# Kernel optimization log

Hardware: AMD Instinct MI355X
Metric: run time of the kernel (lower is better)

The kernel has to match this reference:

```python
import jax, jax.numpy as jnp
import numpy as np
from jax import lax

DIM = 64
HEADS = 8

def conv1x1(x, w):
    # x: [B,C,H,W], w: [O,I,1,1]
    return lax.conv_general_dilated(x, w, (1, 1), 'VALID',
                                    dimension_numbers=('NCHW', 'OIHW', 'NCHW'))

def dwconv3x3(x, w):
    # depthwise 3x3, w: [C,1,3,3]
    C = x.shape[1]
    return lax.conv_general_dilated(x, w, (1, 1), ((1, 1), (1, 1)),
                                    dimension_numbers=('NCHW', 'OIHW', 'NCHW'),
                                    feature_group_count=C)

def setup_inputs() -> dict:
    key = jax.random.key(0)
    ks = jax.random.split(key, 7)
    B, C, H, W = 8, DIM, 256, 256
    x = jax.random.normal(ks[0], (B, C, H, W), dtype=jnp.float32)
    w_gate = jax.random.normal(ks[1], (C, C, 1, 1), dtype=jnp.float32) * 0.05
    w_gate_dw = jax.random.normal(ks[2], (C, 1, 3, 3), dtype=jnp.float32) * 0.05
    w_qkv = jax.random.normal(ks[3], (3 * C, C, 1, 1), dtype=jnp.float32) * 0.05
    w_qkv_dw = jax.random.normal(ks[4], (3 * C, 1, 3, 3), dtype=jnp.float32) * 0.05
    w_proj = jax.random.normal(ks[5], (C, C, 1, 1), dtype=jnp.float32) * 0.05
    temperature = jnp.ones((HEADS, 1, 1), dtype=jnp.float32)
    return {'x': x, 'w_gate': w_gate, 'w_gate_dw': w_gate_dw,
            'w_qkv': w_qkv, 'w_qkv_dw': w_qkv_dw, 'w_proj': w_proj,
            'temperature': temperature}

def reference(x, w_gate, w_gate_dw, w_qkv, w_qkv_dw, w_proj, temperature):
    b, c, h, w = x.shape
    head = HEADS
    cph = c // head  # channels per head

    gate = dwconv3x3(conv1x1(x, w_gate), w_gate_dw)  # [b,c,h,w]
    qkv = dwconv3x3(conv1x1(x, w_qkv), w_qkv_dw)     # [b,3c,h,w]
    q, k, v = jnp.split(qkv, 3, axis=1)

    def to_heads(t):
        return t.reshape(b, head, cph, h * w)  # [b,head,c',hw]
    q, k, v = to_heads(q), to_heads(k), to_heads(v)

    # L2-normalize along the spatial (hw) axis (torch F.normalize, eps=1e-12)
    q = q / jnp.maximum(jnp.linalg.norm(q, axis=-1, keepdims=True), 1e-12)
    k = k / jnp.maximum(jnp.linalg.norm(k, axis=-1, keepdims=True), 1e-12)

    # transposed attention over channels: [b,head,c',c']
    attn = jnp.einsum('bhcn,bhdn->bhcd', q, k) * temperature
    attn = jax.nn.softmax(attn, axis=-1)
    out = jnp.einsum('bhcd,bhdn->bhcn', attn, v)  # [b,head,c',hw]
    out = out.reshape(b, c, h, w)

    out = jax.nn.gelu(gate, approximate=False) * out
    out = conv1x1(out, w_proj)
    return out
```

## Files before the change

kernel.cpp:

```cpp
#include <hip/hip_runtime.h>

typedef _Float16 f16;
using f16x4 = __attribute__((ext_vector_type(4))) _Float16;
using f16x8 = __attribute__((ext_vector_type(8))) _Float16;
using f32x4 = __attribute__((ext_vector_type(4))) float;

#define HW 65536
#define NBAND 16
#define ROWS 16
#define RS 320

static __device__ __forceinline__ float my_erf(float v) {
  float x = fabsf(v);
  float t = 1.f / (1.f + 0.3275911f * x);
  float y = t * (0.254829592f + t * (-0.284496736f + t * (1.421413741f
          + t * (-1.453152027f + t * 1.061405429f))));
  float r = 1.f - y * __expf(-x * x);
  return v < 0.f ? -r : r;
}
static __device__ __forceinline__ float my_gelu(float s) {
  return 0.5f * s * (1.f + my_erf(s * 0.70710678118654752f));
}

__global__ void TRA_Attention_15281493639325_kernel() {}

__global__ void k_signal(float* out, long long n, float val) {
  long long i = (long long)blockIdx.x * blockDim.x + threadIdx.x;
  long long stride = (long long)gridDim.x * blockDim.x;
  for (; i < n; i += stride) out[i] = val;
}

__global__ __launch_bounds__(256) void k0_wconv(
    const float* __restrict__ w_gate, const float* __restrict__ w_qkv,
    f16* __restrict__ W16)
{
  int i = blockIdx.x * 256 + threadIdx.x;
  int m = i >> 4, kc = i & 15;
  const float* src = (m < 64) ? (w_gate + m*64 + kc*4)
                              : (w_qkv + (m-64)*64 + kc*4);
  float4 f = *(const float4*)src;
  f16x4 pk = { (f16)f.x, (f16)f.y, (f16)f.z, (f16)f.w };
  *(f16x4*)(W16 + m*64 + kc*4) = pk;
}

__global__ __launch_bounds__(256) void k1_mfma(
    const float* __restrict__ x, const f16* __restrict__ W16,
    f16* __restrict__ A)
{
  __shared__ __align__(16) unsigned char xs[8192];
  __shared__ __align__(16) f16 os[256*64];

  const int tid = threadIdx.x, blk = blockIdx.x;
  const int b = blk >> 8;
  const long long row0 = (long long)(blk & 255) * 256;

  const int wave = tid >> 6, lane = tid & 63;
  const int m0 = (wave >> 1) * 128, n0 = (wave & 1) * 32;
  const int lr = lane & 15, lg = lane >> 4;

  float4 pre[4];
  #pragma unroll
  for (int i = 0; i < 4; ++i) {
    int cid = tid + (i << 8), k = cid >> 4, c = cid & 15;
    pre[i] = *(const float4*)(x + ((long long)b*64 + k)*HW + row0 + c*4);
  }

  for (int t = 0; t < 4; ++t) {
    const long long p0 = row0 + t*64;

    #pragma unroll
    for (int i = 0; i < 4; ++i) {
      int cid = tid + (i << 8), k = cid >> 4, c = cid & 15;
      const float* e = (const float*)&pre[i];
      #pragma unroll
      for (int j = 0; j < 4; ++j) {
        int p = c*4 + j;
        int hp = ((p & 7) ^ ((p >> 3) & 7)) << 4;
        *(f16*)(xs + p*128 + ((2*k) ^ hp)) = (f16)e[j];
      }
    }
    __syncthreads();

    if (t < 3) {
      const long long pn = row0 + (t+1)*64;
      #pragma unroll
      for (int i = 0; i < 4; ++i) {
        int cid = tid + (i << 8), k = cid >> 4, c = cid & 15;
        pre[i] = *(const float4*)(x + ((long long)b*64 + k)*HW + pn + c*4);
      }
    }

    f32x4 acc[8][2];
    #pragma unroll
    for (int i = 0; i < 8; ++i)
      #pragma unroll
      for (int j = 0; j < 2; ++j) acc[i][j] = (f32x4){0.f,0.f,0.f,0.f};

    #pragma unroll
    for (int ks = 0; ks < 2; ++ks) {
      f16x8 af[8], bfr[2];
      #pragma unroll
      for (int mi = 0; mi < 8; ++mi) {
        int m = m0 + mi*16 + lr;
        af[mi] = *(const f16x8*)(W16 + m*64 + ks*32 + lg*8);
      }
      #pragma unroll
      for (int ni = 0; ni < 2; ++ni) {
        int p = n0 + ni*16 + lr;
        int hp = ((p & 7) ^ ((p >> 3) & 7)) << 4;
        bfr[ni] = *(const f16x8*)(xs + p*128 + ((ks*64 + lg*16) ^ hp));
      }
      #pragma unroll
      for (int mi = 0; mi < 8; ++mi)
        #pragma unroll
        for (int ni = 0; ni < 2; ++ni)
          acc[mi][ni] = __builtin_amdgcn_mfma_f32_16x16x32_f16(
              af[mi], bfr[ni], acc[mi][ni], 0, 0, 0);
    }
    __syncthreads();

    #pragma unroll
    for (int mi = 0; mi < 8; ++mi)
      #pragma unroll
      for (int ni = 0; ni < 2; ++ni)
        #pragma unroll
        for (int r = 0; r < 4; ++r) {
          int m = m0 + mi*16 + lg*4 + r;
          int p = n0 + ni*16 + lr;
          os[m*64 + (p ^ ((m & 7) << 3))] = (f16)acc[mi][ni][r];
        }
    __syncthreads();

    #pragma unroll
    for (int pass = 0; pass < 8; ++pass) {
      int idx = pass*256 + tid;
      int row = idx >> 3, c8 = idx & 7;
      f16x8 v = *(const f16x8*)((const unsigned char*)os + row*128
                                + ((c8 ^ (row & 7)) * 16));
      *(f16x8*)(A + ((long long)b*256 + row)*HW + p0 + c8*8) = v;
    }
    __syncthreads();
  }
}

__global__ __launch_bounds__(256) void k2a_dw(
    const f16* __restrict__ A, const float* __restrict__ w_gate_dw,
    const float* __restrict__ w_qkv_dw, f16* __restrict__ Vv, f16* __restrict__ GG)
{
  const int tid = threadIdx.x, blk = blockIdx.x;
  const int yband = blk & 3, ch2 = (blk >> 2) & 127, b = blk >> 9;
  const bool isv = ch2 >= 64;
  const int c = isv ? ch2 - 64 : ch2;
  const f16* src = A + ((long long)b*256 + (isv ? 192 + c : c)) * HW;
  const float* wsrc = isv ? (w_qkv_dw + (128 + c)*9) : (w_gate_dw + c*9);
  f16* dst = (isv ? Vv : GG) + ((long long)b*64 + c) * HW;

  float wd[9];
  #pragma unroll
  for (int j = 0; j < 9; ++j) wd[j] = wsrc[j];

  const int xc = tid & 31, ysub = tid >> 5;
  const int lane = tid & 63;
  const int xbase = xc * 8;
  const int y0 = yband * 64 + ysub * 8;

  float rb[3][10];

  auto load_row = [&](int y, float* r) {
    if (y >= 0 && y < 256) {
      uint4 raw = *(const uint4*)(src + y*256 + xbase);
      const f16* e = (const f16*)&raw;
      #pragma unroll
      for (int t = 0; t < 8; ++t) r[1 + t] = (float)e[t];
    } else {
      #pragma unroll
      for (int t = 0; t < 8; ++t) r[1 + t] = 0.f;
    }
    float lf = __shfl(r[8], lane - 1);
    float rf = __shfl(r[1], lane + 1);
    r[0] = (xc == 0)  ? 0.f : lf;
    r[9] = (xc == 31) ? 0.f : rf;
  };

  load_row(y0 - 1, rb[0]);
  load_row(y0,     rb[1]);

  #pragma unroll
  for (int i = 0; i < 8; ++i) {
    load_row(y0 + i + 1, rb[(i + 2) % 3]);
    const float* rm = rb[i % 3];
    const float* r0 = rb[(i + 1) % 3];
    const float* rp = rb[(i + 2) % 3];
    f16x8 st;
    #pragma unroll
    for (int j = 0; j < 8; ++j) {
      float s = wd[0]*rm[j] + wd[1]*rm[j+1] + wd[2]*rm[j+2]
              + wd[3]*r0[j] + wd[4]*r0[j+1] + wd[5]*r0[j+2]
              + wd[6]*rp[j] + wd[7]*rp[j+1] + wd[8]*rp[j+2];
      if (!isv) s = my_gelu(s);
      st[j] = (f16)s;
    }
    *(f16x8*)(dst + (y0 + i)*256 + xbase) = st;
  }
}

__device__ __forceinline__ int ridx(int c, int slot, int i) {
  return ((((c << 2) | slot) * RS) + i) ^ ((c & 7) << 3);
}

__global__ __launch_bounds__(64) void k2b_qk(
    const f16* __restrict__ A, const float* __restrict__ w_qkv_dw,
    float* __restrict__ GRP)
{
  __shared__ __align__(16) f16 ring[16*4*RS];
  const int lane = threadIdx.x, blk = blockIdx.x;
  const int band = blk & (NBAND-1), h = (blk >> 4) & 7, b = blk >> 7;

  const int c  = lane & 15, g  = lane >> 4;
  const int cs = lane >> 2, q4 = lane & 3;

  const int wrow = (c < 8) ? (h*8 + c) : (64 + h*8 + (c - 8));
  float wq[9];
  #pragma unroll
  for (int j = 0; j < 9; ++j) wq[j] = w_qkv_dw[wrow*9 + j];

  const f16* sbase = A + ((long long)b*256 +
      (cs < 8 ? 64 + h*8 + cs : 128 + h*8 + (cs - 8))) * HW;

  auto load_row = [&](int yy, uint4* r) {
    if (yy >= 0 && yy < 256) {
      const f16* p = sbase + yy*256 + q4*64;
      #pragma unroll
      for (int t = 0; t < 8; ++t) r[t] = *(const uint4*)(p + t*8);
    } else {
      #pragma unroll
      for (int t = 0; t < 8; ++t) r[t] = make_uint4(0u,0u,0u,0u);
    }
  };
  auto write_row = [&](int slot, const uint4* r) {
    #pragma unroll
    for (int t = 0; t < 8; ++t)
      *(uint4*)&ring[ridx(cs, slot, 8 + q4*64 + t*8)] = r[t];
  };

  auto conv_accum = [&](const f16x8* R, const float* w, float* fr, int q) {
    float v[10];
    #pragma unroll
    for (int t = 0; t < 8; ++t) v[1 + t] = (float)R[q][t];
    float e7p = (q > 0) ? (float)R[q-1][7] : 0.f;
    float e0n = (q < 7) ? (float)R[q+1][0] : 0.f;
    float L1 = __shfl(v[8], lane - 16);
    float L2 = __shfl(e7p, (lane & 15) + 48);
    float Q1 = __shfl(v[1], lane + 16);
    float Q2 = __shfl(e0n, lane & 15);
    v[0] = (g > 0) ? L1 : ((q > 0) ? L2 : 0.f);
    v[9] = (g < 3) ? Q1 : ((q < 7) ? Q2 : 0.f);
    #pragma unroll
    for (int j = 0; j < 8; ++j)
      fr[j] += w[0]*v[j] + w[1]*v[j+1] + w[2]*v[j+2];
  };

  f32x4 acc = (f32x4){0.f, 0.f, 0.f, 0.f};

  const int y0 = band * ROWS;
  {
    uint4 r[8];
    load_row(y0-1, r); write_row((y0+3)&3, r);
    load_row(y0,   r); write_row((y0+4)&3, r);
    load_row(y0+1, r); write_row((y0+5)&3, r);
  }
  __syncthreads();

  for (int y = y0; y < y0 + ROWS; ++y) {
    uint4 r[8];
    const bool pf = (y + 2 <= y0 + ROWS);
    if (pf) load_row(y + 2, r);

    const int s0 = (y+3)&3, s1 = (y+4)&3, s2 = (y+5)&3;
    f16x8 Rm[8], Rc[8], Rp[8];
    #pragma unroll
    for (int q = 0; q < 8; ++q) {
      Rm[q] = *(const f16x8*)&ring[ridx(c, s0, 8 + q*32 + g*8)];
      Rc[q] = *(const f16x8*)&ring[ridx(c, s1, 8 + q*32 + g*8)];
      Rp[q] = *(const f16x8*)&ring[ridx(c, s2, 8 + q*32 + g*8)];
    }

    #pragma unroll
    for (int q = 0; q < 8; ++q) {
      float fr[8] = {0.f,0.f,0.f,0.f,0.f,0.f,0.f,0.f};
      conv_accum(Rm, wq + 0, fr, q);
      conv_accum(Rc, wq + 3, fr, q);
      conv_accum(Rp, wq + 6, fr, q);
      f16x8 frag;
      #pragma unroll
      for (int j = 0; j < 8; ++j) frag[j] = (f16)fr[j];
      acc = __builtin_amdgcn_mfma_f32_16x16x32_f16(frag, frag, acc, 0, 0, 0);
    }

    if (pf) write_row((y+6)&3, r);
    __syncthreads();
  }

  const long long gbase = (long long)((b*8 + h)*NBAND + band) * 80;
  #pragma unroll
  for (int reg = 0; reg < 4; ++reg) {
    int rrow = g*4 + reg;
    float val = acc[reg];
    if (rrow == c) GRP[gbase + c] = val;
    else if (rrow < 8 && c >= 8) GRP[gbase + 16 + rrow*8 + (c-8)] = val;
  }
}

__global__ __launch_bounds__(64) void k2c_attn(
    const float* __restrict__ GRP, const float* __restrict__ temp,
    float* __restrict__ ATT)
{
  __shared__ float s[80];
  const int tid = threadIdx.x;
  const int h = blockIdx.x & 7, b = blockIdx.x >> 3;
  for (int i = tid; i < 80; i += 64) {
    float v = 0.f;
    for (int band = 0; band < NBAND; ++band)
      v += GRP[(((b*8 + h)*NBAND + band) * 80) + i];
    s[i] = v;
  }
  __syncthreads();
  const int c = tid >> 3, d = tid & 7;
  float nq = fmaxf(sqrtf(s[c]), 1e-12f);
  float nk = fmaxf(sqrtf(s[8 + d]), 1e-12f);
  float logit = s[16 + c*8 + d] / (nq * nk) * temp[h];
  float m = logit;
  #pragma unroll
  for (int off = 4; off; off >>= 1) m = fmaxf(m, __shfl_xor(m, off));
  float e = __expf(logit - m);
  float sum = e;
  #pragma unroll
  for (int off = 4; off; off >>= 1) sum += __shfl_xor(sum, off);
  ATT[((b*8 + h)*8 + c)*8 + d] = e / sum;
}

__global__ __launch_bounds__(256) void k3_out(
    const f16* __restrict__ Vv, const f16* __restrict__ GG,
    const float* __restrict__ ATT, const float* __restrict__ w_proj,
    float* __restrict__ out)
{
  __shared__ __align__(16) unsigned char lds[64*128 + 256*128 + 2048];
  unsigned char* wl = lds;
  unsigned char* xs = lds + 64*128;
  float* attn_s = (float*)(lds + 64*128 + 256*128);

  const int tid = threadIdx.x;
  const int y = blockIdx.x & 255, b = blockIdx.x >> 8;

  for (int cid = tid; cid < 1024; cid += 256) {
    int m = cid >> 4, kc = cid & 15;
    float4 f = *(const float4*)(w_proj + m*64 + kc*4);
    int hm = ((m & 7) ^ ((m >> 3) & 7)) << 4;
    f16x4 pk = { (f16)f.x, (f16)f.y, (f16)f.z, (f16)f.w };
    *(f16x4*)(wl + m*128 + ((kc*8) ^ hm)) = pk;
  }
  for (int i = tid; i < 512; i += 256) attn_s[i] = ATT[b*512 + i];
  __syncthreads();

  {
    const int pg = tid & 31, hd = tid >> 5;
    const long long base = ((long long)b*64 + hd*8)*HW + (long long)y*256 + pg*8;
    f16x8 vv[8], gg[8];
    #pragma unroll
    for (int d = 0; d < 8; ++d)
      vv[d] = *(const f16x8*)(Vv + base + (long long)d*HW);
    #pragma unroll
    for (int c = 0; c < 8; ++c)
      gg[c] = *(const f16x8*)(GG + base + (long long)c*HW);
    float a[8][8];
    #pragma unroll
    for (int c = 0; c < 8; ++c)
      #pragma unroll
      for (int d = 0; d < 8; ++d) a[c][d] = attn_s[hd*64 + c*8 + d];
    #pragma unroll
    for (int j = 0; j < 8; ++j) {
      int p = pg*8 + j;
      int hp = ((p & 7) ^ ((p >> 3) & 7)) << 4;
      f16x8 st;
      #pragma unroll
      for (int c = 0; c < 8; ++c) {
        float av = 0.f;
        #pragma unroll
        for (int d = 0; d < 8; ++d) av += a[c][d] * (float)vv[d][j];
        st[c] = (f16)((float)gg[c][j] * av);
      }
      *(f16x8*)(xs + p*128 + ((hd*16) ^ hp)) = st;
    }
  }
  __syncthreads();

  const int wave = tid >> 6, lane = tid & 63;
  const int n0 = wave * 64;
  const int lr = lane & 15, lg = lane >> 4;

  f32x4 acc[4][4];
  #pragma unroll
  for (int i = 0; i < 4; ++i)
    #pragma unroll
    for (int j = 0; j < 4; ++j) acc[i][j] = (f32x4){0.f,0.f,0.f,0.f};

  #pragma unroll
  for (int ks = 0; ks < 2; ++ks) {
    f16x8 af[4], bfr[4];
    #pragma unroll
    for (int mi = 0; mi < 4; ++mi) {
      int m = mi*16 + lr;
      int hm = ((m & 7) ^ ((m >> 3) & 7)) << 4;
      af[mi] = *(const f16x8*)(wl + m*128 + ((ks*64 + lg*16) ^ hm));
    }
    #pragma unroll
    for (int ni = 0; ni < 4; ++ni) {
      int p = n0 + ni*16 + lr;
      int hp = ((p & 7) ^ ((p >> 3) & 7)) << 4;
      bfr[ni] = *(const f16x8*)(xs + p*128 + ((ks*64 + lg*16) ^ hp));
    }
    #pragma unroll
    for (int mi = 0; mi < 4; ++mi)
      #pragma unroll
      for (int ni = 0; ni < 4; ++ni)
        acc[mi][ni] = __builtin_amdgcn_mfma_f32_16x16x32_f16(
            af[mi], bfr[ni], acc[mi][ni], 0, 0, 0);
  }

  const long long obase = (long long)b*64*HW + (long long)y*256;
  #pragma unroll
  for (int mi = 0; mi < 4; ++mi)
    #pragma unroll
    for (int ni = 0; ni < 4; ++ni)
      #pragma unroll
      for (int r = 0; r < 4; ++r) {
        int m = mi*16 + lg*4 + r;
        int p = n0 + ni*16 + lr;
        out[obase + (long long)m*HW + p] = acc[mi][ni][r];
      }
}

extern "C" void kernel_launch(void* const* d_in, const int* in_sizes, int n_in,
                              void* d_out, int out_size, void* d_ws, size_t ws_size,
                              hipStream_t stream)
{
  float* out = (float*)d_out;

  int mp[7] = {-1,-1,-1,-1,-1,-1,-1};
  bool ok = (n_in == 7);
  if (ok) {
    int n4 = 0;
    for (int i = 0; i < 7; ++i) {
      long s = in_sizes[i];
      if      (s == 33554432) mp[0] = i;
      else if (s == 576)      mp[2] = i;
      else if (s == 12288)    mp[3] = i;
      else if (s == 1728)     mp[4] = i;
      else if (s == 8)        mp[6] = i;
      else if (s == 4096)     { if (n4 == 0) mp[1] = i; else mp[5] = i; ++n4; }
    }
    ok = ok && (n4 == 2);
    for (int i = 0; i < 7; ++i) ok = ok && (mp[i] >= 0);
  }
  if (!ok) { k_signal<<<2048,256,0,stream>>>(out, (long long)out_size, 2000.0f); return; }
  if (out_size != 33554432) { k_signal<<<2048,256,0,stream>>>(out, (long long)out_size, 3000.0f); return; }

  const float* x    = (const float*)d_in[mp[0]];
  const float* wg   = (const float*)d_in[mp[1]];
  const float* wgd  = (const float*)d_in[mp[2]];
  const float* wqkv = (const float*)d_in[mp[3]];
  const float* wqd  = (const float*)d_in[mp[4]];
  const float* wpj  = (const float*)d_in[mp[5]];
  const float* tp   = (const float*)d_in[mp[6]];

  unsigned char* ws = (unsigned char*)d_ws;
  const size_t GRP_SZ   = 8UL*8*NBAND*80*4;
  const size_t FULL     = 402653184UL + GRP_SZ + 16384UL + 32768UL;
  const size_t PERB_GRP = 8UL*NBAND*80*4;
  const size_t PERB     = 50331648UL + PERB_GRP + 2048UL + 32768UL;

  if (ws != nullptr && ws_size >= FULL) {
    f16*   A    = (f16*)ws;
    f16*   Vv   = (f16*)(ws + 268435456UL);
    f16*   GG   = (f16*)(ws + 335544320UL);
    float* GRP  = (float*)(ws + 402653184UL);
    float* ATT  = (float*)(ws + 402653184UL + GRP_SZ);
    f16*   W16  = (f16*)(ws + 402653184UL + GRP_SZ + 16384UL);
    k0_wconv<<<16,   256, 0, stream>>>(wg, wqkv, W16);
    k1_mfma <<<2048, 256, 0, stream>>>(x, W16, A);
    k2a_dw  <<<4096, 256, 0, stream>>>(A, wgd, wqd, Vv, GG);
    k2b_qk  <<<8*8*NBAND, 64, 0, stream>>>(A, wqd, GRP);
    k2c_attn<<<64,   64,  0, stream>>>(GRP, tp, ATT);
    k3_out  <<<2048, 256, 0, stream>>>(Vv, GG, ATT, wpj, out);
  } else if (ws != nullptr && ws_size >= PERB) {
    f16*   A    = (f16*)ws;
    f16*   Vv   = (f16*)(ws + 33554432UL);
    f16*   GG   = (f16*)(ws + 41943040UL);
    float* GRP  = (float*)(ws + 50331648UL);
    float* ATT  = (float*)(ws + 50331648UL + PERB_GRP);
    f16*   W16  = (f16*)(ws + 50331648UL + PERB_GRP + 2048UL);
    k0_wconv<<<16, 256, 0, stream>>>(wg, wqkv, W16);
    for (int b = 0; b < 8; ++b) {
      const float* xb = x + (long long)b*64*HW;
      float* ob = out + (long long)b*64*HW;
      k1_mfma <<<256,  256, 0, stream>>>(xb, W16, A);
      k2a_dw  <<<512,  256, 0, stream>>>(A, wgd, wqd, Vv, GG);
      k2b_qk  <<<8*NBAND, 64, 0, stream>>>(A, wqd, GRP);
      k2c_attn<<<8,    64,  0, stream>>>(GRP, tp, ATT);
      k3_out  <<<256,  256, 0, stream>>>(Vv, GG, ATT, wpj, ob);
    }
  } else {
    k_signal<<<2048,256,0,stream>>>(out, (long long)out_size, 1000.0f);
  }
}
```

Before: 270.3 us.

## Fuse depthwise conv for gate and value into the output projection kernel

Removes the separate depthwise-conv kernel that wrote the V and gated G intermediates to global memory. The output kernel now reads the pre-conv channels from A directly, runs the 3x3 depthwise conv on three rows per channel, applies attention and GELU gating in registers, then does the projection. This saves the write and re-read of two 64-channel fp16 tensors. In exchange, each block loads three rows per channel, which leans on cache hits, and keeps more registers live for the accumulators.

```diff
diff --git a/kernel.cpp b/kernel.cpp
--- a/kernel.cpp
+++ b/kernel.cpp
@@ -140,67 +140,6 @@
       *(f16x8*)(A + ((long long)b*256 + row)*HW + p0 + c8*8) = v;
     }
     __syncthreads();
-  }
-}
-
-__global__ __launch_bounds__(256) void k2a_dw(
-    const f16* __restrict__ A, const float* __restrict__ w_gate_dw,
-    const float* __restrict__ w_qkv_dw, f16* __restrict__ Vv, f16* __restrict__ GG)
-{
-  const int tid = threadIdx.x, blk = blockIdx.x;
-  const int yband = blk & 3, ch2 = (blk >> 2) & 127, b = blk >> 9;
-  const bool isv = ch2 >= 64;
-  const int c = isv ? ch2 - 64 : ch2;
-  const f16* src = A + ((long long)b*256 + (isv ? 192 + c : c)) * HW;
-  const float* wsrc = isv ? (w_qkv_dw + (128 + c)*9) : (w_gate_dw + c*9);
-  f16* dst = (isv ? Vv : GG) + ((long long)b*64 + c) * HW;
-
-  float wd[9];
-  #pragma unroll
-  for (int j = 0; j < 9; ++j) wd[j] = wsrc[j];
-
-  const int xc = tid & 31, ysub = tid >> 5;
-  const int lane = tid & 63;
-  const int xbase = xc * 8;
-  const int y0 = yband * 64 + ysub * 8;
-
-  float rb[3][10];
-
-  auto load_row = [&](int y, float* r) {
-    if (y >= 0 && y < 256) {
-      uint4 raw = *(const uint4*)(src + y*256 + xbase);
-      const f16* e = (const f16*)&raw;
-      #pragma unroll
-      for (int t = 0; t < 8; ++t) r[1 + t] = (float)e[t];
-    } else {
-      #pragma unroll
-      for (int t = 0; t < 8; ++t) r[1 + t] = 0.f;
-    }
-    float lf = __shfl(r[8], lane - 1);
-    float rf = __shfl(r[1], lane + 1);
-    r[0] = (xc == 0)  ? 0.f : lf;
-    r[9] = (xc == 31) ? 0.f : rf;
-  };
-
-  load_row(y0 - 1, rb[0]);
-  load_row(y0,     rb[1]);
-
-  #pragma unroll
-  for (int i = 0; i < 8; ++i) {
-    load_row(y0 + i + 1, rb[(i + 2) % 3]);
-    const float* rm = rb[i % 3];
-    const float* r0 = rb[(i + 1) % 3];
-    const float* rp = rb[(i + 2) % 3];
-    f16x8 st;
-    #pragma unroll
-    for (int j = 0; j < 8; ++j) {
-      float s = wd[0]*rm[j] + wd[1]*rm[j+1] + wd[2]*rm[j+2]
-              + wd[3]*r0[j] + wd[4]*r0[j+1] + wd[5]*r0[j+2]
-              + wd[6]*rp[j] + wd[7]*rp[j+1] + wd[8]*rp[j+2];
-      if (!isv) s = my_gelu(s);
-      st[j] = (f16)s;
-    }
-    *(f16x8*)(dst + (y0 + i)*256 + xbase) = st;
   }
 }
 
@@ -339,10 +278,10 @@
   ATT[((b*8 + h)*8 + c)*8 + d] = e / sum;
 }
 
-__global__ __launch_bounds__(256) void k3_out(
-    const f16* __restrict__ Vv, const f16* __restrict__ GG,
-    const float* __restrict__ ATT, const float* __restrict__ w_proj,
-    float* __restrict__ out)
+__global__ __launch_bounds__(256) void k3_fused(
+    const f16* __restrict__ A, const float* __restrict__ ATT,
+    const float* __restrict__ w_gate_dw, const float* __restrict__ w_qkv_dw,
+    const float* __restrict__ w_proj, float* __restrict__ out)
 {
   __shared__ __align__(16) unsigned char lds[64*128 + 256*128 + 2048];
   unsigned char* wl = lds;
@@ -351,6 +290,8 @@
 
   const int tid = threadIdx.x;
   const int y = blockIdx.x & 255, b = blockIdx.x >> 8;
+  const int pg = tid & 31, hd = tid >> 5;
+  const int lane = tid & 63;
 
   for (int cid = tid; cid < 1024; cid += 256) {
     int m = cid >> 4, kc = cid & 15;
@@ -362,39 +303,82 @@
   for (int i = tid; i < 512; i += 256) attn_s[i] = ATT[b*512 + i];
   __syncthreads();
 
-  {
-    const int pg = tid & 31, hd = tid >> 5;
-    const long long base = ((long long)b*64 + hd*8)*HW + (long long)y*256 + pg*8;
-    f16x8 vv[8], gg[8];
-    #pragma unroll
-    for (int d = 0; d < 8; ++d)
-      vv[d] = *(const f16x8*)(Vv + base + (long long)d*HW);
+  auto conv_ch = [&](const f16* chbase, const float* w, float* out8) {
+    uint4 q[3];
+    #pragma unroll
+    for (int rI = 0; rI < 3; ++rI) {
+      int yy = y - 1 + rI;
+      if (yy >= 0 && yy < 256)
+        q[rI] = *(const uint4*)(chbase + yy*256 + pg*8);
+      else
+        q[rI] = make_uint4(0u, 0u, 0u, 0u);
+    }
+    float rr[3][10];
+    #pragma unroll
+    for (int rI = 0; rI < 3; ++rI) {
+      const f16* e = (const f16*)&q[rI];
+      float* r = rr[rI];
+      #pragma unroll
+      for (int t = 0; t < 8; ++t) r[1 + t] = (float)e[t];
+      float lf = __shfl(r[8], lane - 1);
+      float rf = __shfl(r[1], lane + 1);
+      r[0] = (pg == 0)  ? 0.f : lf;
+      r[9] = (pg == 31) ? 0.f : rf;
+    }
+    #pragma unroll
+    for (int j = 0; j < 8; ++j)
+      out8[j] = w[0]*rr[0][j] + w[1]*rr[0][j+1] + w[2]*rr[0][j+2]
+              + w[3]*rr[1][j] + w[4]*rr[1][j+1] + w[5]*rr[1][j+2]
+              + w[6]*rr[2][j] + w[7]*rr[2][j+1] + w[8]*rr[2][j+2];
+  };
+
+  float av[8][8];
+  #pragma unroll
+  for (int c = 0; c < 8; ++c)
+    #pragma unroll
+    for (int j = 0; j < 8; ++j) av[c][j] = 0.f;
+
+  #pragma unroll 2
+  for (int d = 0; d < 8; ++d) {
+    const f16* chb = A + ((long long)b*256 + 192 + hd*8 + d) * HW;
+    float wv[9];
+    #pragma unroll
+    for (int j = 0; j < 9; ++j) wv[j] = w_qkv_dw[(128 + hd*8 + d)*9 + j];
+    float vc[8];
+    conv_ch(chb, wv, vc);
+    float ac[8];
+    #pragma unroll
+    for (int c = 0; c < 8; ++c) ac[c] = attn_s[hd*64 + c*8 + d];
     #pragma unroll
     for (int c = 0; c < 8; ++c)
-      gg[c] = *(const f16x8*)(GG + base + (long long)c*HW);
-    float a[8][8];
-    #pragma unroll
-    for (int c = 0; c < 8; ++c)
-      #pragma unroll
-      for (int d = 0; d < 8; ++d) a[c][d] = attn_s[hd*64 + c*8 + d];
-    #pragma unroll
-    for (int j = 0; j < 8; ++j) {
-      int p = pg*8 + j;
-      int hp = ((p & 7) ^ ((p >> 3) & 7)) << 4;
-      f16x8 st;
-      #pragma unroll
-      for (int c = 0; c < 8; ++c) {
-        float av = 0.f;
-        #pragma unroll
-        for (int d = 0; d < 8; ++d) av += a[c][d] * (float)vv[d][j];
-        st[c] = (f16)((float)gg[c][j] * av);
-      }
-      *(f16x8*)(xs + p*128 + ((hd*16) ^ hp)) = st;
-    }
+      #pragma unroll
+      for (int j = 0; j < 8; ++j) av[c][j] += ac[c] * vc[j];
+  }
+
+  #pragma unroll 2
+  for (int c = 0; c < 8; ++c) {
+    const f16* chb = A + ((long long)b*256 + hd*8 + c) * HW;
+    float wg9[9];
+    #pragma unroll
+    for (int j = 0; j < 9; ++j) wg9[j] = w_gate_dw[(hd*8 + c)*9 + j];
+    float gc[8];
+    conv_ch(chb, wg9, gc);
+    #pragma unroll
+    for (int j = 0; j < 8; ++j) av[c][j] = my_gelu(gc[j]) * av[c][j];
+  }
+
+  #pragma unroll
+  for (int j = 0; j < 8; ++j) {
+    int p = pg*8 + j;
+    int hp = ((p & 7) ^ ((p >> 3) & 7)) << 4;
+    f16x8 st;
+    #pragma unroll
+    for (int c = 0; c < 8; ++c) st[c] = (f16)av[c][j];
+    *(f16x8*)(xs + p*128 + ((hd*16) ^ hp)) = st;
   }
   __syncthreads();
 
-  const int wave = tid >> 6, lane = tid & 63;
+  const int wave = tid >> 6;
   const int n0 = wave * 64;
   const int lr = lane & 15, lg = lane >> 4;
 
@@ -481,21 +465,16 @@
 
   if (ws != nullptr && ws_size >= FULL) {
     f16*   A    = (f16*)ws;
-    f16*   Vv   = (f16*)(ws + 268435456UL);
-    f16*   GG   = (f16*)(ws + 335544320UL);
     float* GRP  = (float*)(ws + 402653184UL);
     float* ATT  = (float*)(ws + 402653184UL + GRP_SZ);
     f16*   W16  = (f16*)(ws + 402653184UL + GRP_SZ + 16384UL);
     k0_wconv<<<16,   256, 0, stream>>>(wg, wqkv, W16);
     k1_mfma <<<2048, 256, 0, stream>>>(x, W16, A);
-    k2a_dw  <<<4096, 256, 0, stream>>>(A, wgd, wqd, Vv, GG);
     k2b_qk  <<<8*8*NBAND, 64, 0, stream>>>(A, wqd, GRP);
     k2c_attn<<<64,   64,  0, stream>>>(GRP, tp, ATT);
-    k3_out  <<<2048, 256, 0, stream>>>(Vv, GG, ATT, wpj, out);
+    k3_fused<<<2048, 256, 0, stream>>>(A, ATT, wgd, wqd, wpj, out);
   } else if (ws != nullptr && ws_size >= PERB) {
     f16*   A    = (f16*)ws;
-    f16*   Vv   = (f16*)(ws + 33554432UL);
-    f16*   GG   = (f16*)(ws + 41943040UL);
     float* GRP  = (float*)(ws + 50331648UL);
     float* ATT  = (float*)(ws + 50331648UL + PERB_GRP);
     f16*   W16  = (f16*)(ws + 50331648UL + PERB_GRP + 2048UL);
@@ -504,10 +483,9 @@
       const float* xb = x + (long long)b*64*HW;
       float* ob = out + (long long)b*64*HW;
       k1_mfma <<<256,  256, 0, stream>>>(xb, W16, A);
-      k2a_dw  <<<512,  256, 0, stream>>>(A, wgd, wqd, Vv, GG);
       k2b_qk  <<<8*NBAND, 64, 0, stream>>>(A, wqd, GRP);
       k2c_attn<<<8,    64,  0, stream>>>(GRP, tp, ATT);
-      k3_out  <<<256,  256, 0, stream>>>(Vv, GG, ATT, wpj, ob);
+      k3_fused<<<256,  256, 0, stream>>>(A, ATT, wgd, wqd, wpj, ob);
     }
   } else {
     k_signal<<<2048,256,0,stream>>>(out, (long long)out_size, 1000.0f);
```

Result: slower. 378.3 us (+39.9%).
